# Optimization experiments

Hardware: AMD Instinct MI355X
Metric: run time of the kernel (lower is better)

Reference implementation:

```python
import jax, jax.numpy as jnp
import numpy as np

KH, KW = 3, 3
PAD = 1


def setup_inputs() -> dict:
    key = jax.random.key(0)
    k1, k2 = jax.random.split(key)
    B, C, H, W = 8, 3, 544, 960
    x = jax.random.normal(k1, (B, C, H, W), dtype=jnp.float32)
    filt = jax.random.uniform(k2, (B, C * KH * KW, H, W), dtype=jnp.float32)
    return {"x": x, "filter": filt}


def _local_expand(x):
    # x: [B, C, H, W] -> [B, C*KH*KW, H, W], channel-major ordering (c slowest)
    B, C, H, W = x.shape
    xp = jnp.pad(x, ((0, 0), (0, 0), (PAD, PAD), (PAD, PAD)))
    patches = jnp.stack(
        [xp[:, :, i:i + H, j:j + W] for i in range(KH) for j in range(KW)],
        axis=2,
    )  # [B, C, KH*KW, H, W]
    return patches.reshape(B, C * KH * KW, H, W)


def reference(x, filter):
    x_le = _local_expand(x)                      # [B, C*k^2, H, W]
    out = jnp.sum(x_le * filter, axis=1, keepdims=True)  # [B, 1, H, W]
    return out
```

## Files before the change

kernel.cpp:

```cpp
#include <hip/hip_runtime.h>

constexpr int B = 8, C = 3, H = 544, W = 960;
constexpr int KH = 3, KW = 3;
constexpr int HW = H * W;
constexpr int WT = 8;
constexpr int WQ = W / WT;
constexpr int NK = C * KH * KW;
constexpr int BLOCK = 256;
constexpr int TOTAL = B * H * WQ;
constexpr int NBLK = TOTAL / BLOCK;
static_assert(TOTAL % BLOCK == 0, "grid must be exact");
static_assert(NBLK % 8 == 0, "swizzle must be bijective");

typedef float f32x4 __attribute__((ext_vector_type(4)));

__global__ __launch_bounds__(BLOCK) void DynFilter_kernel(
    const float* __restrict__ x,
    const float* __restrict__ filt,
    float* __restrict__ out)
{
    int bid  = (int)blockIdx.x;
    int sbid = (bid & 7) * (NBLK / 8) + (bid >> 3);
    int tid  = sbid * BLOCK + (int)threadIdx.x;

    int wq = tid % WQ;
    int t  = tid / WQ;
    int h  = t % H;
    int b  = t / H;
    int w0 = wq * WT;

    f32x4 acc0 = {0.f, 0.f, 0.f, 0.f};
    f32x4 acc1 = {0.f, 0.f, 0.f, 0.f};

    const float* fbase = filt + (size_t)b * NK * HW + (size_t)h * W + w0;

    #pragma unroll
    for (int c = 0; c < C; ++c) {
        const float* xc = x + ((size_t)b * C + c) * HW;
        #pragma unroll
        for (int i = 0; i < KH; ++i) {
            int hr = h + i - 1;
            bool vh = (unsigned)hr < (unsigned)H;
            float xv[WT + 2];
            if (vh) {
                const float* xr = xc + (size_t)hr * W + w0;
                f32x4 m0 = *reinterpret_cast<const f32x4*>(xr);
                f32x4 m1 = *reinterpret_cast<const f32x4*>(xr + 4);
                xv[1] = m0[0]; xv[2] = m0[1]; xv[3] = m0[2]; xv[4] = m0[3];
                xv[5] = m1[0]; xv[6] = m1[1]; xv[7] = m1[2]; xv[8] = m1[3];
                xv[0] = (w0 > 0)      ? xr[-1] : 0.f;
                xv[9] = (w0 + WT < W) ? xr[WT] : 0.f;
            } else {
                #pragma unroll
                for (int q = 0; q < WT + 2; ++q) xv[q] = 0.f;
            }
            #pragma unroll
            for (int j = 0; j < KW; ++j) {
                int k = c * (KH * KW) + i * KW + j;
                const float* fp = fbase + (size_t)k * HW;
                f32x4 f0 = __builtin_nontemporal_load(reinterpret_cast<const f32x4*>(fp));
                f32x4 f1 = __builtin_nontemporal_load(reinterpret_cast<const f32x4*>(fp) + 1);
                acc0[0] += xv[j]     * f0[0];
                acc0[1] += xv[j + 1] * f0[1];
                acc0[2] += xv[j + 2] * f0[2];
                acc0[3] += xv[j + 3] * f0[3];
                acc1[0] += xv[j + 4] * f1[0];
                acc1[1] += xv[j + 5] * f1[1];
                acc1[2] += xv[j + 6] * f1[2];
                acc1[3] += xv[j + 7] * f1[3];
            }
        }
    }

    float* op = out + (size_t)b * HW + (size_t)h * W + w0;
    __builtin_nontemporal_store(acc0, reinterpret_cast<f32x4*>(op));
    __builtin_nontemporal_store(acc1, reinterpret_cast<f32x4*>(op) + 1);
}

extern "C" void kernel_launch(void* const* d_in, const int* in_sizes, int n_in,
                              void* d_out, int out_size, void* d_ws, size_t ws_size,
                              hipStream_t stream) {
    const float* x    = (const float*)d_in[0];
    const float* filt = (const float*)d_in[1];
    float* out        = (float*)d_out;

    DynFilter_kernel<<<NBLK, BLOCK, 0, stream>>>(x, filt, out);
}
```

Baseline: 104.7 us.

## Compute two output rows per thread to reuse input rows across taps

Each thread now produces a 2x8 output tile, loading four input rows per channel instead of three rows per output row, so the x row loads are shared between the two outputs. The block-index swizzle is removed and the filter loads switch from nontemporal to normal loads. This halves the thread count and raises registers per thread, and may change how filter traffic behaves in the caches. The kernel is dominated by the filter stream, so the gain from fewer x loads is limited.

```diff
diff --git a/kernel.cpp b/kernel.cpp
--- a/kernel.cpp
+++ b/kernel.cpp
@@ -4,77 +4,92 @@
 constexpr int KH = 3, KW = 3;
 constexpr int HW = H * W;
 constexpr int WT = 8;
+constexpr int HT = 2;
 constexpr int WQ = W / WT;
+constexpr int HG = H / HT;
 constexpr int NK = C * KH * KW;
 constexpr int BLOCK = 256;
-constexpr int TOTAL = B * H * WQ;
+constexpr int TOTAL = B * HG * WQ;
 constexpr int NBLK = TOTAL / BLOCK;
 static_assert(TOTAL % BLOCK == 0, "grid must be exact");
-static_assert(NBLK % 8 == 0, "swizzle must be bijective");
 
 typedef float f32x4 __attribute__((ext_vector_type(4)));
+
+__device__ __forceinline__ void load_row(const float* xr, bool valid,
+                                         bool left, bool right,
+                                         float xv[WT + 2]) {
+    if (valid) {
+        f32x4 m0 = *reinterpret_cast<const f32x4*>(xr);
+        f32x4 m1 = *reinterpret_cast<const f32x4*>(xr + 4);
+        xv[1] = m0[0]; xv[2] = m0[1]; xv[3] = m0[2]; xv[4] = m0[3];
+        xv[5] = m1[0]; xv[6] = m1[1]; xv[7] = m1[2]; xv[8] = m1[3];
+        xv[0] = left  ? xr[-1] : 0.f;
+        xv[9] = right ? xr[WT] : 0.f;
+    } else {
+        #pragma unroll
+        for (int q = 0; q < WT + 2; ++q) xv[q] = 0.f;
+    }
+}
 
 __global__ __launch_bounds__(BLOCK) void DynFilter_kernel(
     const float* __restrict__ x,
     const float* __restrict__ filt,
     float* __restrict__ out)
 {
-    int bid  = (int)blockIdx.x;
-    int sbid = (bid & 7) * (NBLK / 8) + (bid >> 3);
-    int tid  = sbid * BLOCK + (int)threadIdx.x;
+    int tid = (int)blockIdx.x * BLOCK + (int)threadIdx.x;
 
     int wq = tid % WQ;
     int t  = tid / WQ;
-    int h  = t % H;
-    int b  = t / H;
+    int hg = t % HG;
+    int b  = t / HG;
+    int h0 = hg * HT;
     int w0 = wq * WT;
+    bool left  = (w0 > 0);
+    bool right = (w0 + WT < W);
 
-    f32x4 acc0 = {0.f, 0.f, 0.f, 0.f};
-    f32x4 acc1 = {0.f, 0.f, 0.f, 0.f};
+    f32x4 a00 = {0,0,0,0}, a01 = {0,0,0,0};
+    f32x4 a10 = {0,0,0,0}, a11 = {0,0,0,0};
 
-    const float* fbase = filt + (size_t)b * NK * HW + (size_t)h * W + w0;
+    const float* fbase = filt + (size_t)b * NK * HW + (size_t)h0 * W + w0;
 
     #pragma unroll
     for (int c = 0; c < C; ++c) {
         const float* xc = x + ((size_t)b * C + c) * HW;
+
+        float xva[WT + 2], xvb[WT + 2], xvc[WT + 2], xvd[WT + 2];
+        load_row(xc + (size_t)(h0 - 1) * W + w0, h0 > 0,     left, right, xva);
+        load_row(xc + (size_t)(h0    ) * W + w0, true,       left, right, xvb);
+        load_row(xc + (size_t)(h0 + 1) * W + w0, true,       left, right, xvc);
+        load_row(xc + (size_t)(h0 + 2) * W + w0, h0 + 2 < H, left, right, xvd);
+
         #pragma unroll
         for (int i = 0; i < KH; ++i) {
-            int hr = h + i - 1;
-            bool vh = (unsigned)hr < (unsigned)H;
-            float xv[WT + 2];
-            if (vh) {
-                const float* xr = xc + (size_t)hr * W + w0;
-                f32x4 m0 = *reinterpret_cast<const f32x4*>(xr);
-                f32x4 m1 = *reinterpret_cast<const f32x4*>(xr + 4);
-                xv[1] = m0[0]; xv[2] = m0[1]; xv[3] = m0[2]; xv[4] = m0[3];
-                xv[5] = m1[0]; xv[6] = m1[1]; xv[7] = m1[2]; xv[8] = m1[3];
-                xv[0] = (w0 > 0)      ? xr[-1] : 0.f;
-                xv[9] = (w0 + WT < W) ? xr[WT] : 0.f;
-            } else {
-                #pragma unroll
-                for (int q = 0; q < WT + 2; ++q) xv[q] = 0.f;
-            }
+            const float* r0 = (i == 0) ? xva : (i == 1) ? xvb : xvc;
+            const float* r1 = (i == 0) ? xvb : (i == 1) ? xvc : xvd;
             #pragma unroll
             for (int j = 0; j < KW; ++j) {
                 int k = c * (KH * KW) + i * KW + j;
                 const float* fp = fbase + (size_t)k * HW;
-                f32x4 f0 = __builtin_nontemporal_load(reinterpret_cast<const f32x4*>(fp));
-                f32x4 f1 = __builtin_nontemporal_load(reinterpret_cast<const f32x4*>(fp) + 1);
-                acc0[0] += xv[j]     * f0[0];
-                acc0[1] += xv[j + 1] * f0[1];
-                acc0[2] += xv[j + 2] * f0[2];
-                acc0[3] += xv[j + 3] * f0[3];
-                acc1[0] += xv[j + 4] * f1[0];
-                acc1[1] += xv[j + 5] * f1[1];
-                acc1[2] += xv[j + 6] * f1[2];
-                acc1[3] += xv[j + 7] * f1[3];
+                f32x4 g0 = *reinterpret_cast<const f32x4*>(fp);
+                f32x4 g1 = *reinterpret_cast<const f32x4*>(fp + 4);
+                f32x4 g2 = *reinterpret_cast<const f32x4*>(fp + W);
+                f32x4 g3 = *reinterpret_cast<const f32x4*>(fp + W + 4);
+                #pragma unroll
+                for (int q = 0; q < 4; ++q) {
+                    a00[q] += r0[j + q]     * g0[q];
+                    a01[q] += r0[j + q + 4] * g1[q];
+                    a10[q] += r1[j + q]     * g2[q];
+                    a11[q] += r1[j + q + 4] * g3[q];
+                }
             }
         }
     }
 
-    float* op = out + (size_t)b * HW + (size_t)h * W + w0;
-    __builtin_nontemporal_store(acc0, reinterpret_cast<f32x4*>(op));
-    __builtin_nontemporal_store(acc1, reinterpret_cast<f32x4*>(op) + 1);
+    float* op = out + (size_t)b * HW + (size_t)h0 * W + w0;
+    __builtin_nontemporal_store(a00, reinterpret_cast<f32x4*>(op));
+    __builtin_nontemporal_store(a01, reinterpret_cast<f32x4*>(op) + 1);
+    __builtin_nontemporal_store(a10, reinterpret_cast<f32x4*>(op + W));
+    __builtin_nontemporal_store(a11, reinterpret_cast<f32x4*>(op + W) + 1);
 }
 
 extern "C" void kernel_launch(void* const* d_in, const int* in_sizes, int n_in,
```

Result: faster. 92.75 us (median of 2 runs) (-11.4%).
